# Performance work log

Measured on AMD Instinct MI355X. Metric: run time of the kernel, lower is better.

The kernel has to match this reference:

```python
import jax, jax.numpy as jnp
import numpy as np

EPS = 1e-9
SECOND_THRESHOLD = 0.2     # train threshold
CAPACITY_FACTOR = 1.25     # train capacity factor
MIN_EXPERT_CAPACITY = 4


def setup_inputs() -> dict:
    key = jax.random.key(0)
    k1, k2, k3 = jax.random.split(key, 3)
    x = jax.random.normal(k1, (8, 2048, 1024), dtype=jnp.float32)
    w_gating = jax.random.normal(k2, (1024, 64), dtype=jnp.float32)
    noise = jax.random.uniform(k3, (8, 2048), dtype=jnp.float32)  # replaces torch uniform_ probs
    return {"x": x, "w_gating": w_gating, "noise": noise}


def reference(x, w_gating, noise):
    b, n, d = x.shape
    e = w_gating.shape[-1]

    gate_logits = jnp.einsum('bnd,de->bne', x, w_gating)          # [b,n,e]
    raw_gates = jax.nn.softmax(gate_logits, axis=-1)

    top_vals, top_idx = jax.lax.top_k(raw_gates, 2)               # [b,n,2]
    gate_1, gate_2 = top_vals[..., 0], top_vals[..., 1]
    index_1, index_2 = top_idx[..., 0], top_idx[..., 1]
    mask_1 = jax.nn.one_hot(index_1, e, dtype=jnp.float32)        # [b,n,e]
    mask_2 = jax.nn.one_hot(index_2, e, dtype=jnp.float32)

    denom = gate_1 + gate_2 + EPS
    gate_1 = gate_1 / denom
    gate_2 = gate_2 / denom

    # load-balance loss (training path)
    density_1 = mask_1.mean(axis=-2)                              # [b,e]
    density_1_proxy = raw_gates.mean(axis=-2)
    balance_loss = (density_1_proxy * density_1).mean() * float(e * e)

    # stochastic second-expert routing
    route_second = (noise < gate_2 / max(SECOND_THRESHOLD, EPS)).astype(jnp.float32)
    mask_2 = mask_2 * route_second[..., None]

    expert_capacity = max(min(n, int(n * CAPACITY_FACTOR / e)), MIN_EXPERT_CAPACITY)
    cap_f = float(expert_capacity)

    # exclusive cumsum along token dim: cumsum(t) - t
    position_in_expert_1 = (jnp.cumsum(mask_1, axis=-2) - mask_1) * mask_1
    mask_1 = mask_1 * (position_in_expert_1 < cap_f).astype(jnp.float32)
    mask_1_count = mask_1.mean(axis=-2, keepdims=True)            # NOTE: mean, as in source
    mask_1_flat = mask_1.sum(axis=-1)                             # [b,n]
    position_in_expert_1 = position_in_expert_1.sum(axis=-1)      # [b,n]
    gate_1 = gate_1 * mask_1_flat

    position_in_expert_2 = (jnp.cumsum(mask_2, axis=-2) - mask_2 + mask_1_count) * mask_2
    mask_2 = mask_2 * (position_in_expert_2 < cap_f).astype(jnp.float32)
    mask_2_flat = mask_2.sum(axis=-1)
    position_in_expert_2 = position_in_expert_2.sum(axis=-1)
    gate_2 = gate_2 * mask_2_flat

    oh_e1 = jax.nn.one_hot(index_1, e, dtype=jnp.float32)         # [b,n,e]
    oh_e2 = jax.nn.one_hot(index_2, e, dtype=jnp.float32)
    oh_p1 = jax.nn.one_hot(position_in_expert_1.astype(jnp.int32), expert_capacity, dtype=jnp.float32)  # [b,n,cap]
    oh_p2 = jax.nn.one_hot(position_in_expert_2.astype(jnp.int32), expert_capacity, dtype=jnp.float32)

    combine_tensor = (
        (gate_1 * mask_1_flat)[..., None, None] * oh_e1[..., :, None] * oh_p1[..., None, :]
        + (gate_2 * mask_2_flat)[..., None, None] * oh_e2[..., :, None] * oh_p2[..., None, :]
    )                                                             # [b,n,e,cap]

    dispatch_tensor = jax.lax.stop_gradient((combine_tensor != 0).astype(x.dtype))

    router_z_loss = jnp.mean(jnp.square(jax.nn.logsumexp(gate_logits, axis=-1)))

    return dispatch_tensor, combine_tensor, balance_loss, router_z_loss
```

## Files before the change

### kernel.cpp

```cpp
#include <hip/hip_runtime.h>
#include <cstdint>
#include <cstddef>

#define NB 8
#define NTOK 2048
#define TOKENS (NB * NTOK)
#define D 1024
#define E 64
#define CAP 40
#define EC (E * CAP)
#define OUT_TENSOR ((size_t)TOKENS * EC)
#define CHUNKS 32
#define CHTOK 64

#define TOTAL_F4 20971520ull
#define S2 14745600ull

typedef __attribute__((ext_vector_type(8))) short short8v;
typedef __attribute__((ext_vector_type(4))) float f32x4;

__device__ __forceinline__ unsigned short f2bf(float f) {
  unsigned u = __float_as_uint(f);
  unsigned r = (u + 0x7FFFu + ((u >> 16) & 1u)) >> 16;
  return (unsigned short)r;
}

__device__ __forceinline__ void nt_zero(float4* p) {
  __builtin_nontemporal_store((f32x4){0.f, 0.f, 0.f, 0.f},
                              reinterpret_cast<f32x4*>(p));
}

__global__ __launch_bounds__(256) void k_prep(const float* __restrict__ w,
                                              unsigned short* __restrict__ wT,
                                              float* __restrict__ proxyacc) {
  int gid = blockIdx.x * 256 + threadIdx.x;
  int e = gid >> 10, k = gid & 1023;
  wT[gid] = f2bf(w[k * E + e]);
  if (blockIdx.x == 0) {
    proxyacc[threadIdx.x] = 0.f;
    proxyacc[threadIdx.x + 256] = 0.f;
  }
}

__global__ __launch_bounds__(256, 1) void k_gemmgate_fill(const float* __restrict__ x,
                                                          const unsigned short* __restrict__ wT,
                                                          const float* __restrict__ noise,
                                                          int* __restrict__ i1o, int* __restrict__ i2o,
                                                          float* __restrict__ g1o, float* __restrict__ g2o,
                                                          float* __restrict__ proxyacc,
                                                          float* __restrict__ zpart,
                                                          float* __restrict__ out) {
  const int tid = threadIdx.x;

  if (blockIdx.x >= 256) {
    float4* o4 = reinterpret_cast<float4*>(out);
    size_t q = (size_t)(blockIdx.x - 256) * 256 + tid;
#pragma unroll 5
    for (int i = 0; i < 75; ++i, q += 768 * 256) nt_zero(&o4[q]);
    return;
  }

  const int m0 = blockIdx.x * 64;
  const int l = tid & 63;
  const int wv = tid >> 6;
  const int h = l >> 4;
  const int r = l & 15;

  const float* xrow = x + (size_t)(m0 + 16 * wv + r) * D;
  const unsigned short* wr0 = wT + (size_t)(r) * D;
  const unsigned short* wr1 = wT + (size_t)(16 + r) * D;
  const unsigned short* wr2 = wT + (size_t)(32 + r) * D;
  const unsigned short* wr3 = wT + (size_t)(48 + r) * D;

  f32x4 acc[4];
#pragma unroll
  for (int f = 0; f < 4; ++f) acc[f] = (f32x4){0.f, 0.f, 0.f, 0.f};

  f32x4 ua[2][2], va[2][2];
  short8v bb[2][2][4];

#define LOAD(BUF, C)                                                   \
  {                                                                    \
    _Pragma("unroll") for (int s = 0; s < 2; ++s) {                    \
      const int k0 = 64 * (C) + 32 * s + 8 * h;                        \
      ua[BUF][s] = *(const f32x4*)(xrow + k0);                         \
      va[BUF][s] = *(const f32x4*)(xrow + k0 + 4);                     \
      bb[BUF][s][0] = *(const short8v*)(wr0 + k0);                     \
      bb[BUF][s][1] = *(const short8v*)(wr1 + k0);                     \
      bb[BUF][s][2] = *(const short8v*)(wr2 + k0);                     \
      bb[BUF][s][3] = *(const short8v*)(wr3 + k0);                     \
    }                                                                  \
  }

  LOAD(0, 0);
#pragma unroll
  for (int c = 0; c < 16; ++c) {
    const int cur = c & 1;
    if (c < 15) LOAD((c + 1) & 1, c + 1);
#pragma unroll
    for (int s = 0; s < 2; ++s) {
      f32x4 u = ua[cur][s];
      f32x4 v = va[cur][s];
      short8v av;
      av[0] = (short)f2bf(u.x); av[1] = (short)f2bf(u.y);
      av[2] = (short)f2bf(u.z); av[3] = (short)f2bf(u.w);
      av[4] = (short)f2bf(v.x); av[5] = (short)f2bf(v.y);
      av[6] = (short)f2bf(v.z); av[7] = (short)f2bf(v.w);
#pragma unroll
      for (int f = 0; f < 4; ++f)
        acc[f] = __builtin_amdgcn_mfma_f32_16x16x32_bf16(av, bb[cur][s][f], acc[f], 0, 0, 0);
    }
  }
#undef LOAD

  const int bslot = (m0 >> 11) * E;
  float pxl0 = 0.f, pxl1 = 0.f, pxl2 = 0.f, pxl3 = 0.f;
  float zw = 0.f;
  int c1a[4], c2a[4];
  float g1a[4], g2a[4];
  bool routea[4];

#pragma unroll
  for (int rr = 0; rr < 4; ++rr) {
    float l0 = acc[0][rr], l1 = acc[1][rr], l2 = acc[2][rr], l3 = acc[3][rr];
    float m = fmaxf(fmaxf(l0, l1), fmaxf(l2, l3));
#pragma unroll
    for (int off = 1; off < 16; off <<= 1) m = fmaxf(m, __shfl_xor(m, off));
    float p0 = expf(l0 - m), p1 = expf(l1 - m), p2 = expf(l2 - m), p3 = expf(l3 - m);
    float s = p0 + p1 + p2 + p3;
#pragma unroll
    for (int off = 1; off < 16; off <<= 1) s += __shfl_xor(s, off);

    float m1 = fmaxf(fmaxf(p0, p1), fmaxf(p2, p3));
#pragma unroll
    for (int off = 1; off < 16; off <<= 1) m1 = fmaxf(m1, __shfl_xor(m1, off));
    int lidx = 999;
    if (p0 == m1) lidx = r;
    if (p1 == m1) lidx = min(lidx, 16 + r);
    if (p2 == m1) lidx = min(lidx, 32 + r);
    if (p3 == m1) lidx = min(lidx, 48 + r);
#pragma unroll
    for (int off = 1; off < 16; off <<= 1) lidx = min(lidx, __shfl_xor(lidx, off));
    int c1 = lidx;

    float q0 = (c1 == r) ? -1.f : p0;
    float q1 = (c1 == 16 + r) ? -1.f : p1;
    float q2 = (c1 == 32 + r) ? -1.f : p2;
    float q3 = (c1 == 48 + r) ? -1.f : p3;
    float m2 = fmaxf(fmaxf(q0, q1), fmaxf(q2, q3));
#pragma unroll
    for (int off = 1; off < 16; off <<= 1) m2 = fmaxf(m2, __shfl_xor(m2, off));
    int lidx2 = 999;
    if (q0 == m2) lidx2 = r;
    if (q1 == m2) lidx2 = min(lidx2, 16 + r);
    if (q2 == m2) lidx2 = min(lidx2, 32 + r);
    if (q3 == m2) lidx2 = min(lidx2, 48 + r);
#pragma unroll
    for (int off = 1; off < 16; off <<= 1) lidx2 = min(lidx2, __shfl_xor(lidx2, off));
    int c2 = lidx2;

    float g1 = m1 / s;
    float g2 = m2 / s;
    float denom = g1 + g2 + 1e-9f;
    float g1n = g1 / denom;
    float g2n = g2 / denom;
    int token = m0 + 16 * wv + 4 * h + rr;
    bool route = noise[token] < (g2n / 0.2f);

    c1a[rr] = c1; c2a[rr] = c2; g1a[rr] = g1n; g2a[rr] = g2n; routea[rr] = route;

    pxl0 += p0 / s; pxl1 += p1 / s; pxl2 += p2 / s; pxl3 += p3 / s;
    float lse = m + logf(s);
    zw += lse * lse;
  }

  if (r == 0) {
#pragma unroll
    for (int rr = 0; rr < 4; ++rr) {
      int token = m0 + 16 * wv + 4 * h + rr;
      i1o[token] = c1a[rr];
      i2o[token] = routea[rr] ? c2a[rr] : -1;
      g1o[token] = g1a[rr];
      g2o[token] = g2a[rr];
    }
  }

  pxl0 += __shfl_xor(pxl0, 16); pxl0 += __shfl_xor(pxl0, 32);
  pxl1 += __shfl_xor(pxl1, 16); pxl1 += __shfl_xor(pxl1, 32);
  pxl2 += __shfl_xor(pxl2, 16); pxl2 += __shfl_xor(pxl2, 32);
  pxl3 += __shfl_xor(pxl3, 16); pxl3 += __shfl_xor(pxl3, 32);
  if (l < 16) {
    atomicAdd(&proxyacc[bslot + r], pxl0);
    atomicAdd(&proxyacc[bslot + 16 + r], pxl1);
    atomicAdd(&proxyacc[bslot + 32 + r], pxl2);
    atomicAdd(&proxyacc[bslot + 48 + r], pxl3);
  }
  zw += __shfl_xor(zw, 16); zw += __shfl_xor(zw, 32);
  if (l == 0) zpart[blockIdx.x * 4 + wv] = zw;
}

__global__ __launch_bounds__(1024) void k_pos_fill(const int* __restrict__ i1,
                                                   const int* __restrict__ i2r,
                                                   const float* __restrict__ g1,
                                                   const float* __restrict__ g2,
                                                   int4* __restrict__ tokinfo,
                                                   int* __restrict__ count1,
                                                   float* __restrict__ out) {
  if (blockIdx.x >= NB) {
    const size_t fi = (size_t)blockIdx.x - NB;
    float4* o4 = reinterpret_cast<float4*>(out);
    for (size_t q = S2 + fi * 1024 + threadIdx.x; q < TOTAL_F4; q += (size_t)512 * 1024)
      nt_zero(&o4[q]);
    return;
  }
  __shared__ unsigned char pos1c[NTOK];
  __shared__ unsigned char pos2c[NTOK];
  __shared__ int cnt1[CHUNKS][E];
  __shared__ int cnt2[CHUNKS][E];

  const int b = blockIdx.x;
  const int tid = threadIdx.x;
  const int wave = tid >> 6;
  const int lane = tid & 63;
  const unsigned long long lt = (lane == 63) ? 0x7FFFFFFFFFFFFFFFull
                                             : ((1ull << lane) - 1ull);

#pragma unroll
  for (int ci = 0; ci < 2; ++ci) {
    const int c = wave * 2 + ci;
    const int base = c * CHTOK;
    int e1 = i1[b * NTOK + base + lane];
    int e2 = i2r[b * NTOK + base + lane];
    int p1 = 0, p2 = 0, myc1 = 0, myc2 = 0;
    for (int e = 0; e < E; ++e) {
      unsigned long long m1 = __ballot(e1 == e);
      unsigned long long m2 = __ballot(e2 == e);
      if (e1 == e) p1 = __popcll(m1 & lt);
      if (e2 == e) p2 = __popcll(m2 & lt);
      if (lane == e) { myc1 = __popcll(m1); myc2 = __popcll(m2); }
    }
    pos1c[base + lane] = (unsigned char)p1;
    pos2c[base + lane] = (unsigned char)p2;
    cnt1[c][lane] = myc1;
    cnt2[c][lane] = myc2;
  }
  __syncthreads();

  if (tid < E) {
    int run1 = 0, run2 = 0;
#pragma unroll 4
    for (int c = 0; c < CHUNKS; ++c) {
      int v1 = cnt1[c][tid]; cnt1[c][tid] = run1; run1 += v1;
      int v2 = cnt2[c][tid]; cnt2[c][tid] = run2; run2 += v2;
    }
    count1[b * E + tid] = run1;
  }
  __syncthreads();

#pragma unroll
  for (int ci = 0; ci < 2; ++ci) {
    const int c = wave * 2 + ci;
    const int base = c * CHTOK;
    const int t = b * NTOK + base + lane;
    int e1 = i1[t];
    int e2 = i2r[t];
    int pp1 = cnt1[c][e1] + (int)pos1c[base + lane];
    int w1 = (pp1 < CAP) ? e1 * CAP + pp1 : -1;
    int w2 = -1;
    if (e2 >= 0) {
      int pp2 = cnt2[c][e2] + (int)pos2c[base + lane];
      if (pp2 < CAP) w2 = e2 * CAP + pp2;
    }
    tokinfo[t] = make_int4(w1, w2, __float_as_int(g1[t]), __float_as_int(g2[t]));
  }
}

__global__ __launch_bounds__(256) void k_scatter_final(const int4* __restrict__ tokinfo,
                                                       const float* __restrict__ zpart,
                                                       const float* __restrict__ proxyacc,
                                                       const int* __restrict__ count1,
                                                       float* __restrict__ out) {
  const int t = blockIdx.x * 256 + threadIdx.x;
  const int tid = threadIdx.x;
  if (t < TOKENS) {
    int4 ti = tokinfo[t];
    float* dispatch = out;
    float* combine = out + OUT_TENSOR;
    if (ti.x >= 0) {
      size_t off = (size_t)t * EC + ti.x;
      combine[off] = __int_as_float(ti.z);
      dispatch[off] = 1.f;
    }
    if (ti.y >= 0) {
      size_t off = (size_t)t * EC + ti.y;
      combine[off] = __int_as_float(ti.w);
      dispatch[off] = 1.f;
    }
  }

  if (blockIdx.x == 0) {
    __shared__ float red[256];
    float zs = 0.f;
    for (int i = tid; i < 1024; i += 256) zs += zpart[i];
    red[tid] = zs;
    __syncthreads();
    for (int s = 128; s > 0; s >>= 1) {
      if (tid < s) red[tid] += red[tid + s];
      __syncthreads();
    }
    float ztot = red[0];
    __syncthreads();
    float bs = 0.f;
    for (int i = tid; i < 512; i += 256) bs += proxyacc[i] * (float)count1[i];
    red[tid] = bs;
    __syncthreads();
    for (int s = 128; s > 0; s >>= 1) {
      if (tid < s) red[tid] += red[tid + s];
      __syncthreads();
    }
    if (tid == 0) {
      out[2 * OUT_TENSOR] = red[0] / 524288.f;
      out[2 * OUT_TENSOR + 1] = ztot / 16384.f;
    }
  }
}

extern "C" void kernel_launch(void* const* d_in, const int* in_sizes, int n_in,
                              void* d_out, int out_size, void* d_ws, size_t ws_size,
                              hipStream_t stream) {
  const float* x = (const float*)d_in[0];
  const float* w = (const float*)d_in[1];
  const float* noise = (const float*)d_in[2];
  float* out = (float*)d_out;

  float* ws = (float*)d_ws;
  int* i1 = (int*)ws;
  int* i2r = i1 + TOKENS;
  float* g1 = (float*)(i2r + TOKENS);
  float* g2 = g1 + TOKENS;
  float* proxyacc = g2 + TOKENS;
  int* count1 = (int*)(proxyacc + 512);
  float* zpart = (float*)(count1 + 512);
  unsigned short* wT = (unsigned short*)(zpart + 1024);
  int4* tokinfo = (int4*)((float*)wT + 32768);

  k_prep<<<256, 256, 0, stream>>>(w, wT, proxyacc);
  k_gemmgate_fill<<<1024, 256, 0, stream>>>(x, wT, noise, i1, i2r, g1, g2,
                                            proxyacc, zpart, out);
  k_pos_fill<<<NB + 512, 1024, 0, stream>>>(i1, i2r, g1, g2, tokinfo, count1, out);
  k_scatter_final<<<64, 256, 0, stream>>>(tokinfo, zpart, proxyacc, count1, out);
}
```

Baseline: 87.80 us.

## Move all output zero-fill into GEMM kernel and scatter directly from position kernel

The zero-fill of the dispatch/combine tensors was split between the GEMM kernel and the position kernel. Now the GEMM kernel's extra blocks zero the whole output, and the position kernel no longer fills. The position kernel writes the scatter entries itself instead of going through a tokinfo buffer and a separate scatter kernel. This drops one intermediate buffer round trip and changes how the memory-bound fill overlaps with the compute-bound GEMM, at the cost of a longer fill tail in the GEMM launch and only 8 blocks doing the scatter.

```diff
diff --git a/kernel.cpp b/kernel.cpp
--- a/kernel.cpp
+++ b/kernel.cpp
@@ -14,7 +14,6 @@
 #define CHTOK 64
 
 #define TOTAL_F4 20971520ull
-#define S2 14745600ull
 
 typedef __attribute__((ext_vector_type(8))) short short8v;
 typedef __attribute__((ext_vector_type(4))) float f32x4;
@@ -54,9 +53,9 @@
 
   if (blockIdx.x >= 256) {
     float4* o4 = reinterpret_cast<float4*>(out);
-    size_t q = (size_t)(blockIdx.x - 256) * 256 + tid;
-#pragma unroll 5
-    for (int i = 0; i < 75; ++i, q += 768 * 256) nt_zero(&o4[q]);
+    const size_t stride = 768 * 256;
+    for (size_t q = (size_t)(blockIdx.x - 256) * 256 + tid; q < TOTAL_F4; q += stride)
+      nt_zero(&o4[q]);
     return;
   }
 
@@ -199,20 +198,12 @@
   if (l == 0) zpart[blockIdx.x * 4 + wv] = zw;
 }
 
-__global__ __launch_bounds__(1024) void k_pos_fill(const int* __restrict__ i1,
-                                                   const int* __restrict__ i2r,
-                                                   const float* __restrict__ g1,
-                                                   const float* __restrict__ g2,
-                                                   int4* __restrict__ tokinfo,
-                                                   int* __restrict__ count1,
-                                                   float* __restrict__ out) {
-  if (blockIdx.x >= NB) {
-    const size_t fi = (size_t)blockIdx.x - NB;
-    float4* o4 = reinterpret_cast<float4*>(out);
-    for (size_t q = S2 + fi * 1024 + threadIdx.x; q < TOTAL_F4; q += (size_t)512 * 1024)
-      nt_zero(&o4[q]);
-    return;
-  }
+__global__ __launch_bounds__(1024) void k_pos_scatter(const int* __restrict__ i1,
+                                                      const int* __restrict__ i2r,
+                                                      const float* __restrict__ g1,
+                                                      const float* __restrict__ g2,
+                                                      int* __restrict__ count1,
+                                                      float* __restrict__ out) {
   __shared__ unsigned char pos1c[NTOK];
   __shared__ unsigned char pos2c[NTOK];
   __shared__ int cnt1[CHUNKS][E];
@@ -257,6 +248,7 @@
   }
   __syncthreads();
 
+  float* combine = out + OUT_TENSOR;
 #pragma unroll
   for (int ci = 0; ci < 2; ++ci) {
     const int c = wave * 2 + ci;
@@ -265,63 +257,49 @@
     int e1 = i1[t];
     int e2 = i2r[t];
     int pp1 = cnt1[c][e1] + (int)pos1c[base + lane];
-    int w1 = (pp1 < CAP) ? e1 * CAP + pp1 : -1;
-    int w2 = -1;
+    if (pp1 < CAP) {
+      size_t off = (size_t)t * EC + e1 * CAP + pp1;
+      combine[off] = g1[t];
+      out[off] = 1.f;
+    }
     if (e2 >= 0) {
       int pp2 = cnt2[c][e2] + (int)pos2c[base + lane];
-      if (pp2 < CAP) w2 = e2 * CAP + pp2;
-    }
-    tokinfo[t] = make_int4(w1, w2, __float_as_int(g1[t]), __float_as_int(g2[t]));
-  }
-}
-
-__global__ __launch_bounds__(256) void k_scatter_final(const int4* __restrict__ tokinfo,
-                                                       const float* __restrict__ zpart,
-                                                       const float* __restrict__ proxyacc,
-                                                       const int* __restrict__ count1,
-                                                       float* __restrict__ out) {
-  const int t = blockIdx.x * 256 + threadIdx.x;
+      if (pp2 < CAP) {
+        size_t off = (size_t)t * EC + e2 * CAP + pp2;
+        combine[off] = g2[t];
+        out[off] = 1.f;
+      }
+    }
+  }
+}
+
+__global__ __launch_bounds__(256) void k_final(const float* __restrict__ zpart,
+                                               const float* __restrict__ proxyacc,
+                                               const int* __restrict__ count1,
+                                               float* __restrict__ out) {
   const int tid = threadIdx.x;
-  if (t < TOKENS) {
-    int4 ti = tokinfo[t];
-    float* dispatch = out;
-    float* combine = out + OUT_TENSOR;
-    if (ti.x >= 0) {
-      size_t off = (size_t)t * EC + ti.x;
-      combine[off] = __int_as_float(ti.z);
-      dispatch[off] = 1.f;
-    }
-    if (ti.y >= 0) {
-      size_t off = (size_t)t * EC + ti.y;
-      combine[off] = __int_as_float(ti.w);
-      dispatch[off] = 1.f;
-    }
-  }
-
-  if (blockIdx.x == 0) {
-    __shared__ float red[256];
-    float zs = 0.f;
-    for (int i = tid; i < 1024; i += 256) zs += zpart[i];
-    red[tid] = zs;
+  __shared__ float red[256];
+  float zs = 0.f;
+  for (int i = tid; i < 1024; i += 256) zs += zpart[i];
+  red[tid] = zs;
+  __syncthreads();
+  for (int s = 128; s > 0; s >>= 1) {
+    if (tid < s) red[tid] += red[tid + s];
     __syncthreads();
-    for (int s = 128; s > 0; s >>= 1) {
-      if (tid < s) red[tid] += red[tid + s];
-      __syncthreads();
-    }
-    float ztot = red[0];
+  }
+  float ztot = red[0];
+  __syncthreads();
+  float bs = 0.f;
+  for (int i = tid; i < 512; i += 256) bs += proxyacc[i] * (float)count1[i];
+  red[tid] = bs;
+  __syncthreads();
+  for (int s = 128; s > 0; s >>= 1) {
+    if (tid < s) red[tid] += red[tid + s];
     __syncthreads();
-    float bs = 0.f;
-    for (int i = tid; i < 512; i += 256) bs += proxyacc[i] * (float)count1[i];
-    red[tid] = bs;
-    __syncthreads();
-    for (int s = 128; s > 0; s >>= 1) {
-      if (tid < s) red[tid] += red[tid + s];
-      __syncthreads();
-    }
-    if (tid == 0) {
-      out[2 * OUT_TENSOR] = red[0] / 524288.f;
-      out[2 * OUT_TENSOR + 1] = ztot / 16384.f;
-    }
+  }
+  if (tid == 0) {
+    out[2 * OUT_TENSOR] = red[0] / 524288.f;
+    out[2 * OUT_TENSOR + 1] = ztot / 16384.f;
   }
 }
 
@@ -342,11 +320,10 @@
   int* count1 = (int*)(proxyacc + 512);
   float* zpart = (float*)(count1 + 512);
   unsigned short* wT = (unsigned short*)(zpart + 1024);
-  int4* tokinfo = (int4*)((float*)wT + 32768);
 
   k_prep<<<256, 256, 0, stream>>>(w, wT, proxyacc);
   k_gemmgate_fill<<<1024, 256, 0, stream>>>(x, wT, noise, i1, i2r, g1, g2,
                                             proxyacc, zpart, out);
-  k_pos_fill<<<NB + 512, 1024, 0, stream>>>(i1, i2r, g1, g2, tokinfo, count1, out);
-  k_scatter_final<<<64, 256, 0, stream>>>(tokinfo, zpart, proxyacc, count1, out);
-}
+  k_pos_scatter<<<NB, 1024, 0, stream>>>(i1, i2r, g1, g2, count1, out);
+  k_final<<<1, 256, 0, stream>>>(zpart, proxyacc, count1, out);
+}
```

New measurement: 98.36 us. +12.0%, slower.

## Fuse four kernels into two using flag-based inter-block synchronization

Applied to the files above, without the earlier changes.

The weight transpose/convert kernel is folded into the GEMM+gate kernel: zero-fill blocks also write the bf16 transposed weights and publish per-block release flags, which the GEMM blocks spin on after issuing their first x loads. The position and scatter kernels are merged: 8 blocks compute positions with 256 threads each, 512 blocks zero-fill, and the remaining blocks wait on an atomic counter before scattering and computing the losses. This removes two launches and the gaps between them. In exchange it relies on co-residency to avoid deadlock and leaves fewer threads on the position-scan critical path. The flags are never reset, so later calls can read wT before it is rewritten.

```diff
diff --git a/kernel.cpp b/kernel.cpp
--- a/kernel.cpp
+++ b/kernel.cpp
@@ -15,6 +15,7 @@
 
 #define TOTAL_F4 20971520ull
 #define S2 14745600ull
+#define MAGIC 0x5A17ED42
 
 typedef __attribute__((ext_vector_type(8))) short short8v;
 typedef __attribute__((ext_vector_type(4))) float f32x4;
@@ -30,47 +31,48 @@
                               reinterpret_cast<f32x4*>(p));
 }
 
-__global__ __launch_bounds__(256) void k_prep(const float* __restrict__ w,
-                                              unsigned short* __restrict__ wT,
-                                              float* __restrict__ proxyacc) {
-  int gid = blockIdx.x * 256 + threadIdx.x;
-  int e = gid >> 10, k = gid & 1023;
-  wT[gid] = f2bf(w[k * E + e]);
-  if (blockIdx.x == 0) {
-    proxyacc[threadIdx.x] = 0.f;
-    proxyacc[threadIdx.x + 256] = 0.f;
-  }
-}
-
-__global__ __launch_bounds__(256, 1) void k_gemmgate_fill(const float* __restrict__ x,
-                                                          const unsigned short* __restrict__ wT,
-                                                          const float* __restrict__ noise,
-                                                          int* __restrict__ i1o, int* __restrict__ i2o,
-                                                          float* __restrict__ g1o, float* __restrict__ g2o,
-                                                          float* __restrict__ proxyacc,
-                                                          float* __restrict__ zpart,
-                                                          float* __restrict__ out) {
+__global__ __launch_bounds__(256, 1) void k_gemmgate_prep_fill(
+    const float* __restrict__ x, const float* __restrict__ w,
+    const unsigned short* __restrict__ wTc,
+    unsigned short* __restrict__ wT,
+    const float* __restrict__ noise,
+    int* __restrict__ i1o, int* __restrict__ i2o,
+    float* __restrict__ g1o, float* __restrict__ g2o,
+    float* __restrict__ proxyacc, float* __restrict__ zpart,
+    int* __restrict__ flags, int* __restrict__ ctr2,
+    float* __restrict__ out) {
+  const int bid = blockIdx.x;
   const int tid = threadIdx.x;
 
-  if (blockIdx.x >= 256) {
+  if (bid >= 256) {
+    if (bid < 512) {
+      int gid = (bid - 256) * 256 + tid;
+      int e = gid >> 10, k = gid & 1023;
+      wT[gid] = f2bf(w[k * E + e]);
+      if (bid == 256) proxyacc[tid] = 0.f;
+      if (bid == 257) proxyacc[256 + tid] = 0.f;
+      __threadfence();
+      __syncthreads();
+      if (tid == 0)
+        __hip_atomic_store(&flags[bid - 256], MAGIC, __ATOMIC_RELEASE,
+                           __HIP_MEMORY_SCOPE_AGENT);
+    }
     float4* o4 = reinterpret_cast<float4*>(out);
-    size_t q = (size_t)(blockIdx.x - 256) * 256 + tid;
-#pragma unroll 5
-    for (int i = 0; i < 75; ++i, q += 768 * 256) nt_zero(&o4[q]);
+    const size_t stride = 768 * 256;
+    for (size_t q = (size_t)(bid - 256) * 256 + tid; q < S2; q += stride)
+      nt_zero(&o4[q]);
     return;
   }
 
-  const int m0 = blockIdx.x * 64;
+  if (bid == 0 && tid == 0) *ctr2 = 0;
+
+  const int m0 = bid * 64;
   const int l = tid & 63;
   const int wv = tid >> 6;
   const int h = l >> 4;
   const int r = l & 15;
 
   const float* xrow = x + (size_t)(m0 + 16 * wv + r) * D;
-  const unsigned short* wr0 = wT + (size_t)(r) * D;
-  const unsigned short* wr1 = wT + (size_t)(16 + r) * D;
-  const unsigned short* wr2 = wT + (size_t)(32 + r) * D;
-  const unsigned short* wr3 = wT + (size_t)(48 + r) * D;
 
   f32x4 acc[4];
 #pragma unroll
@@ -79,12 +81,18 @@
   f32x4 ua[2][2], va[2][2];
   short8v bb[2][2][4];
 
-#define LOAD(BUF, C)                                                   \
+#define LOADA(BUF, C)                                                  \
   {                                                                    \
     _Pragma("unroll") for (int s = 0; s < 2; ++s) {                    \
       const int k0 = 64 * (C) + 32 * s + 8 * h;                        \
       ua[BUF][s] = *(const f32x4*)(xrow + k0);                         \
       va[BUF][s] = *(const f32x4*)(xrow + k0 + 4);                     \
+    }                                                                  \
+  }
+#define LOADB(BUF, C)                                                  \
+  {                                                                    \
+    _Pragma("unroll") for (int s = 0; s < 2; ++s) {                    \
+      const int k0 = 64 * (C) + 32 * s + 8 * h;                        \
       bb[BUF][s][0] = *(const short8v*)(wr0 + k0);                     \
       bb[BUF][s][1] = *(const short8v*)(wr1 + k0);                     \
       bb[BUF][s][2] = *(const short8v*)(wr2 + k0);                     \
@@ -92,11 +100,23 @@
     }                                                                  \
   }
 
-  LOAD(0, 0);
+  LOADA(0, 0);
+
+  while (__hip_atomic_load(&flags[tid], __ATOMIC_ACQUIRE,
+                           __HIP_MEMORY_SCOPE_AGENT) != MAGIC)
+    __builtin_amdgcn_s_sleep(2);
+  __syncthreads();
+
+  const unsigned short* wr0 = wTc + (size_t)(r) * D;
+  const unsigned short* wr1 = wTc + (size_t)(16 + r) * D;
+  const unsigned short* wr2 = wTc + (size_t)(32 + r) * D;
+  const unsigned short* wr3 = wTc + (size_t)(48 + r) * D;
+
+  LOADB(0, 0);
 #pragma unroll
   for (int c = 0; c < 16; ++c) {
     const int cur = c & 1;
-    if (c < 15) LOAD((c + 1) & 1, c + 1);
+    if (c < 15) { LOADA((c + 1) & 1, c + 1); LOADB((c + 1) & 1, c + 1); }
 #pragma unroll
     for (int s = 0; s < 2; ++s) {
       f32x4 u = ua[cur][s];
@@ -111,7 +131,8 @@
         acc[f] = __builtin_amdgcn_mfma_f32_16x16x32_bf16(av, bb[cur][s][f], acc[f], 0, 0, 0);
     }
   }
-#undef LOAD
+#undef LOADA
+#undef LOADB
 
   const int bslot = (m0 >> 11) * E;
   float pxl0 = 0.f, pxl1 = 0.f, pxl2 = 0.f, pxl3 = 0.f;
@@ -196,93 +217,104 @@
     atomicAdd(&proxyacc[bslot + 48 + r], pxl3);
   }
   zw += __shfl_xor(zw, 16); zw += __shfl_xor(zw, 32);
-  if (l == 0) zpart[blockIdx.x * 4 + wv] = zw;
-}
-
-__global__ __launch_bounds__(1024) void k_pos_fill(const int* __restrict__ i1,
-                                                   const int* __restrict__ i2r,
-                                                   const float* __restrict__ g1,
-                                                   const float* __restrict__ g2,
-                                                   int4* __restrict__ tokinfo,
-                                                   int* __restrict__ count1,
-                                                   float* __restrict__ out) {
-  if (blockIdx.x >= NB) {
-    const size_t fi = (size_t)blockIdx.x - NB;
+  if (l == 0) zpart[bid * 4 + wv] = zw;
+}
+
+__global__ __launch_bounds__(256) void k_pos_fill_scatter(
+    const int* __restrict__ i1, const int* __restrict__ i2r,
+    const float* __restrict__ g1, const float* __restrict__ g2,
+    int4* __restrict__ tokinfo, int* __restrict__ count1,
+    const float* __restrict__ zpart, const float* __restrict__ proxyacc,
+    int* __restrict__ ctr2, float* __restrict__ out) {
+  const int bid = blockIdx.x;
+  const int tid = threadIdx.x;
+
+  if (bid >= 8 && bid < 520) {
     float4* o4 = reinterpret_cast<float4*>(out);
-    for (size_t q = S2 + fi * 1024 + threadIdx.x; q < TOTAL_F4; q += (size_t)512 * 1024)
+    const size_t stride = 512 * 256;
+    for (size_t q = S2 + (size_t)(bid - 8) * 256 + tid; q < TOTAL_F4; q += stride)
       nt_zero(&o4[q]);
+    __threadfence();
+    __syncthreads();
+    if (tid == 0) atomicAdd(ctr2, 1);
     return;
   }
-  __shared__ unsigned char pos1c[NTOK];
-  __shared__ unsigned char pos2c[NTOK];
-  __shared__ int cnt1[CHUNKS][E];
-  __shared__ int cnt2[CHUNKS][E];
-
-  const int b = blockIdx.x;
-  const int tid = threadIdx.x;
-  const int wave = tid >> 6;
-  const int lane = tid & 63;
-  const unsigned long long lt = (lane == 63) ? 0x7FFFFFFFFFFFFFFFull
-                                             : ((1ull << lane) - 1ull);
-
-#pragma unroll
-  for (int ci = 0; ci < 2; ++ci) {
-    const int c = wave * 2 + ci;
-    const int base = c * CHTOK;
-    int e1 = i1[b * NTOK + base + lane];
-    int e2 = i2r[b * NTOK + base + lane];
-    int p1 = 0, p2 = 0, myc1 = 0, myc2 = 0;
-    for (int e = 0; e < E; ++e) {
-      unsigned long long m1 = __ballot(e1 == e);
-      unsigned long long m2 = __ballot(e2 == e);
-      if (e1 == e) p1 = __popcll(m1 & lt);
-      if (e2 == e) p2 = __popcll(m2 & lt);
-      if (lane == e) { myc1 = __popcll(m1); myc2 = __popcll(m2); }
-    }
-    pos1c[base + lane] = (unsigned char)p1;
-    pos2c[base + lane] = (unsigned char)p2;
-    cnt1[c][lane] = myc1;
-    cnt2[c][lane] = myc2;
+
+  if (bid < 8) {
+    __shared__ unsigned char pos1c[NTOK];
+    __shared__ unsigned char pos2c[NTOK];
+    __shared__ int cnt1[CHUNKS][E];
+    __shared__ int cnt2[CHUNKS][E];
+
+    const int b = bid;
+    const int wave = tid >> 6;
+    const int lane = tid & 63;
+    const unsigned long long lt = (lane == 63) ? 0x7FFFFFFFFFFFFFFFull
+                                               : ((1ull << lane) - 1ull);
+
+#pragma unroll
+    for (int ci = 0; ci < 8; ++ci) {
+      const int c = wave * 8 + ci;
+      const int base = c * CHTOK;
+      int e1 = i1[b * NTOK + base + lane];
+      int e2 = i2r[b * NTOK + base + lane];
+      int p1 = 0, p2 = 0, myc1 = 0, myc2 = 0;
+      for (int e = 0; e < E; ++e) {
+        unsigned long long m1 = __ballot(e1 == e);
+        unsigned long long m2 = __ballot(e2 == e);
+        if (e1 == e) p1 = __popcll(m1 & lt);
+        if (e2 == e) p2 = __popcll(m2 & lt);
+        if (lane == e) { myc1 = __popcll(m1); myc2 = __popcll(m2); }
+      }
+      pos1c[base + lane] = (unsigned char)p1;
+      pos2c[base + lane] = (unsigned char)p2;
+      cnt1[c][lane] = myc1;
+      cnt2[c][lane] = myc2;
+    }
+    __syncthreads();
+
+    if (tid < E) {
+      int run1 = 0, run2 = 0;
+#pragma unroll 4
+      for (int c = 0; c < CHUNKS; ++c) {
+        int v1 = cnt1[c][tid]; cnt1[c][tid] = run1; run1 += v1;
+        int v2 = cnt2[c][tid]; cnt2[c][tid] = run2; run2 += v2;
+      }
+      count1[b * E + tid] = run1;
+    }
+    __syncthreads();
+
+#pragma unroll
+    for (int ci = 0; ci < 8; ++ci) {
+      const int c = wave * 8 + ci;
+      const int base = c * CHTOK;
+      const int t = b * NTOK + base + lane;
+      int e1 = i1[t];
+      int e2 = i2r[t];
+      int pp1 = cnt1[c][e1] + (int)pos1c[base + lane];
+      int w1 = (pp1 < CAP) ? e1 * CAP + pp1 : -1;
+      int w2 = -1;
+      if (e2 >= 0) {
+        int pp2 = cnt2[c][e2] + (int)pos2c[base + lane];
+        if (pp2 < CAP) w2 = e2 * CAP + pp2;
+      }
+      tokinfo[t] = make_int4(w1, w2, __float_as_int(g1[t]), __float_as_int(g2[t]));
+    }
+    __threadfence();
+    __syncthreads();
+    if (tid == 0) atomicAdd(ctr2, 1);
+    return;
+  }
+
+  if (tid == 0) {
+    while (__hip_atomic_load(ctr2, __ATOMIC_ACQUIRE,
+                             __HIP_MEMORY_SCOPE_AGENT) != 520)
+      __builtin_amdgcn_s_sleep(2);
   }
   __syncthreads();
 
-  if (tid < E) {
-    int run1 = 0, run2 = 0;
-#pragma unroll 4
-    for (int c = 0; c < CHUNKS; ++c) {
-      int v1 = cnt1[c][tid]; cnt1[c][tid] = run1; run1 += v1;
-      int v2 = cnt2[c][tid]; cnt2[c][tid] = run2; run2 += v2;
-    }
-    count1[b * E + tid] = run1;
-  }
-  __syncthreads();
-
-#pragma unroll
-  for (int ci = 0; ci < 2; ++ci) {
-    const int c = wave * 2 + ci;
-    const int base = c * CHTOK;
-    const int t = b * NTOK + base + lane;
-    int e1 = i1[t];
-    int e2 = i2r[t];
-    int pp1 = cnt1[c][e1] + (int)pos1c[base + lane];
-    int w1 = (pp1 < CAP) ? e1 * CAP + pp1 : -1;
-    int w2 = -1;
-    if (e2 >= 0) {
-      int pp2 = cnt2[c][e2] + (int)pos2c[base + lane];
-      if (pp2 < CAP) w2 = e2 * CAP + pp2;
-    }
-    tokinfo[t] = make_int4(w1, w2, __float_as_int(g1[t]), __float_as_int(g2[t]));
-  }
-}
-
-__global__ __launch_bounds__(256) void k_scatter_final(const int4* __restrict__ tokinfo,
-                                                       const float* __restrict__ zpart,
-                                                       const float* __restrict__ proxyacc,
-                                                       const int* __restrict__ count1,
-                                                       float* __restrict__ out) {
-  const int t = blockIdx.x * 256 + threadIdx.x;
-  const int tid = threadIdx.x;
-  if (t < TOKENS) {
+  const int t = (bid - 520) * 256 + tid;
+  {
     int4 ti = tokinfo[t];
     float* dispatch = out;
     float* combine = out + OUT_TENSOR;
@@ -298,7 +330,7 @@
     }
   }
 
-  if (blockIdx.x == 0) {
+  if (bid == 520) {
     __shared__ float red[256];
     float zs = 0.f;
     for (int i = tid; i < 1024; i += 256) zs += zpart[i];
@@ -343,10 +375,12 @@
   float* zpart = (float*)(count1 + 512);
   unsigned short* wT = (unsigned short*)(zpart + 1024);
   int4* tokinfo = (int4*)((float*)wT + 32768);
-
-  k_prep<<<256, 256, 0, stream>>>(w, wT, proxyacc);
-  k_gemmgate_fill<<<1024, 256, 0, stream>>>(x, wT, noise, i1, i2r, g1, g2,
-                                            proxyacc, zpart, out);
-  k_pos_fill<<<NB + 512, 1024, 0, stream>>>(i1, i2r, g1, g2, tokinfo, count1, out);
-  k_scatter_final<<<64, 256, 0, stream>>>(tokinfo, zpart, proxyacc, count1, out);
-}
+  int* flags = (int*)(tokinfo + TOKENS);
+  int* ctr2 = flags + 256;
+
+  k_gemmgate_prep_fill<<<1024, 256, 0, stream>>>(x, w, wT, wT, noise, i1, i2r,
+                                                 g1, g2, proxyacc, zpart,
+                                                 flags, ctr2, out);
+  k_pos_fill_scatter<<<584, 256, 0, stream>>>(i1, i2r, g1, g2, tokinfo, count1,
+                                              zpart, proxyacc, ctr2, out);
+}
```

Result: slower. 182.8 us (+108.2%).
